# Kernel tuning notes

Measured on AMD Instinct MI355X. Metric: run time of the kernel, lower is better.

The kernel has to match this reference:

```python
import jax, jax.numpy as jnp
import numpy as np

C = 64


def setup_inputs() -> dict:
    key = jax.random.key(0)
    ks = jax.random.split(key, 7)
    x = jax.random.normal(ks[0], (8, C, 64, 64), dtype=jnp.float32)
    # 1x1 conv weights stored as [out_c, in_c]; biases [out_c]
    s = 1.0 / np.sqrt(C)
    W1 = jax.random.uniform(ks[1], (C, C), jnp.float32, -s, s)
    b1 = jax.random.uniform(ks[2], (C,), jnp.float32, -s, s)
    W2 = jax.random.uniform(ks[3], (C, C), jnp.float32, -s, s)
    b2 = jax.random.uniform(ks[4], (C,), jnp.float32, -s, s)
    W3 = jax.random.uniform(ks[5], (C, C), jnp.float32, -s, s)
    b3 = jax.random.uniform(ks[6], (C,), jnp.float32, -s, s)
    return {"x": x, "W1": W1, "b1": b1, "W2": W2, "b2": b2, "W3": W3, "b3": b3}


def reference(x, W1, b1, W2, b2, W3, b3):
    gamma = 1.0
    b, c, h, w = x.shape
    xf = x.reshape(b, c, h * w)  # [b, c, n]
    # 1x1 convs == per-pixel channel matmuls
    f = jnp.einsum('oc,bcn->bon', W1, xf) + b1[None, :, None]
    g = jnp.einsum('oc,bcn->bon', W2, xf) + b2[None, :, None]
    k = jnp.einsum('oc,bcn->bon', W3, xf) + b3[None, :, None]
    # scores[b,i,j] = sum_c f[b,c,i] * g[b,c,j]; softmax over j
    scores = jnp.einsum('bci,bcj->bij', f, g)
    attn = jax.nn.softmax(scores, axis=2)
    # out_attn[b,c,i] = sum_j attn[b,i,j] * k[b,c,j]
    out = jnp.einsum('bij,bcj->bci', attn, k).reshape(b, c, h, w)
    return gamma * out + x
```

## Files before the change

kernel.cpp:

```cpp
#include <hip/hip_runtime.h>
#include <hip/hip_bf16.h>

#define NPIX 4096
#define CCH  64
#define NB   8
#define KVBLK 64

typedef __attribute__((ext_vector_type(8)))  short short8;
typedef __attribute__((ext_vector_type(4)))  float f32x4;
typedef __attribute__((ext_vector_type(16))) float f32x16;

#define LOG2E   1.44269504f

__device__ __forceinline__ unsigned int pack_bf16(float lo, float hi) {
    union { __hip_bfloat162 h; unsigned int u; } w;
    w.h = __float22bfloat162_rn(make_float2(lo, hi));
    return w.u;
}

__global__ __launch_bounds__(256) void proj_kernel(
    const float* __restrict__ x,
    const float* __restrict__ W1, const float* __restrict__ b1,
    const float* __restrict__ W2, const float* __restrict__ b2,
    const float* __restrict__ W3, const float* __restrict__ b3,
    __hip_bfloat16* __restrict__ Q, __hip_bfloat16* __restrict__ G,
    __hip_bfloat16* __restrict__ K)
{
    const int b    = blockIdx.x >> 6;
    const int i0   = (blockIdx.x & 63) << 6;
    const int tid  = threadIdx.x;
    const int wave = tid >> 6;
    const int lane = tid & 63;
    const int l32  = lane & 31;
    const int hi   = lane >> 5;

    __shared__ __hip_bfloat16 Xt[64][72];
    __shared__ __hip_bfloat16 Wb[3][64][64];
    __shared__ float bsh[3][64];

    for (int e = tid; e < 1024; e += 256) {
        const int c = e >> 4, p4 = (e & 15) * 4;
        const f32x4 v = *(const f32x4*)&x[((size_t)b * CCH + c) * NPIX + i0 + p4];
        #pragma unroll
        for (int t = 0; t < 4; ++t)
            Xt[p4 + t][c] = __float2bfloat16(v[t]);
    }
    #pragma unroll
    for (int m = 0; m < 3; ++m) {
        const float* W = (m == 0) ? W1 : (m == 1) ? W2 : W3;
        for (int e = tid; e < 1024; e += 256) {
            const int oc = e >> 4, c4 = (e & 15) * 4;
            const f32x4 v = *(const f32x4*)&W[oc * 64 + c4];
            *(unsigned int*)&Wb[m][oc][c4]     = pack_bf16(v[0], v[1]);
            *(unsigned int*)&Wb[m][oc][c4 + 2] = pack_bf16(v[2], v[3]);
        }
    }
    if (tid < 192) {
        const int m = tid >> 6, oc = tid & 63;
        bsh[m][oc] = ((m == 0) ? b1 : (m == 1) ? b2 : b3)[oc];
    }
    __syncthreads();

    #pragma unroll
    for (int u = 0; u < 3; ++u) {
        const int unit = wave + 4 * u;
        const int m  = unit >> 2;
        const int sr = (unit >> 1) & 1;
        const int sc = unit & 1;

        f32x16 acc;
        #pragma unroll
        for (int r = 0; r < 16; ++r) {
            const int oc = sr * 32 + (r & 3) + 8 * (r >> 2) + 4 * hi;
            acc[r] = bsh[m][oc];
        }
        #pragma unroll
        for (int ks = 0; ks < 4; ++ks) {
            const short8 af = *(const short8*)&Wb[m][sr * 32 + l32][ks * 16 + hi * 8];
            const short8 bf = *(const short8*)&Xt[sc * 32 + l32][ks * 16 + hi * 8];
            acc = __builtin_amdgcn_mfma_f32_32x32x16_bf16(af, bf, acc, 0, 0, 0);
        }

        const int i = i0 + sc * 32 + l32;
        if (m == 0) {
            #pragma unroll
            for (int r = 0; r < 16; ++r) {
                const int oc = sr * 32 + (r & 3) + 8 * (r >> 2) + 4 * hi;
                Q[((size_t)b * NPIX + i) * CCH + oc] = __float2bfloat16(acc[r] * LOG2E);
            }
        } else if (m == 1) {
            #pragma unroll
            for (int r = 0; r < 16; ++r) {
                const int oc = sr * 32 + (r & 3) + 8 * (r >> 2) + 4 * hi;
                G[((size_t)b * NPIX + i) * CCH + oc] = __float2bfloat16(acc[r]);
            }
        } else {
            #pragma unroll
            for (int r = 0; r < 16; ++r) {
                const int oc = sr * 32 + (r & 3) + 8 * (r >> 2) + 4 * hi;
                K[((size_t)b * CCH + oc) * NPIX + i] = __float2bfloat16(acc[r]);
            }
        }
    }
}

__device__ __forceinline__ void gload_lds16(const void* g, void* l) {
    __builtin_amdgcn_global_load_lds(
        (const __attribute__((address_space(1))) unsigned int*)g,
        (__attribute__((address_space(3))) unsigned int*)l, 16, 0, 0);
}

__global__ __launch_bounds__(512, 4) void attn_kernel(
    const __hip_bfloat16* __restrict__ Qg, const __hip_bfloat16* __restrict__ Gg,
    const __hip_bfloat16* __restrict__ Kg,
    __hip_bfloat16* __restrict__ Opart, float* __restrict__ Lpart, int split)
{
    __shared__ char lds[2][16384];

    const int blk   = blockIdx.x;
    const int per_b = 16 * split;
    const int b     = blk / per_b;
    const int rem   = blk - b * per_b;
    const int itile = rem / split;
    const int sp    = rem - itile * split;
    const int tid   = threadIdx.x;
    const int wave  = tid >> 6;
    const int lane  = tid & 63;
    const int l32   = lane & 31;
    const int hi    = lane >> 5;
    const int i0w   = itile * 256 + wave * 32;
    const int jcnt  = NPIX / split;
    const int jlo   = sp * jcnt;
    const int niter = jcnt / KVBLK;

    const short* Qb = (const short*)Qg + (size_t)b * NPIX * CCH;
    const char*  Gb = (const char*)(Gg + (size_t)b * NPIX * CCH);
    const char*  Kb = (const char*)(Kg + (size_t)b * CCH * NPIX);

    short8 q[4];
    #pragma unroll
    for (int ks = 0; ks < 4; ++ks)
        q[ks] = *(const short8*)(Qb + (size_t)(i0w + l32) * CCH + ks * 16 + hi * 8);

    int gbase[2], kbase[2];
    #pragma unroll
    for (int jb = 0; jb < 2; ++jb)
        gbase[jb] = (jb * 32 + l32) * 128 + ((l32 & 7) << 4);
    #pragma unroll
    for (int cb = 0; cb < 2; ++cb)
        kbase[cb] = 8192 + (cb * 32 + l32) * 128 + ((l32 & 7) << 4);

    const int srow = tid >> 3, scolb = (tid & 7) * 16;
    const char* gsrc = Gb + (size_t)(jlo + srow) * 128 + (scolb ^ ((srow & 7) << 4));
    const char* ksrc = Kb + (size_t)srow * 8192 + (size_t)jlo * 2 + (scolb ^ ((srow & 7) << 4));

    f32x16 zacc;
    #pragma unroll
    for (int r = 0; r < 16; ++r) zacc[r] = 0.f;

    f32x16 o[2];
    #pragma unroll
    for (int cb = 0; cb < 2; ++cb)
        #pragma unroll
        for (int r = 0; r < 16; ++r) o[cb][r] = 0.f;
    float ps = 0.f;

    auto STAGE = [&](int buf, int tt) {
        gload_lds16(gsrc + tt * (KVBLK * 128), lds[buf] + wave * 1024);
        gload_lds16(ksrc + tt * (KVBLK * 2),  lds[buf] + 8192 + wave * 1024);
    };

    STAGE(0, 0);
    __syncthreads();

    for (int t = 0; t < niter; ++t) {
        const int cur = t & 1;
        STAGE(cur ^ 1, (t + 1 < niter) ? t + 1 : 0);
        const char* L = lds[cur];

        #pragma unroll
        for (int jb = 0; jb < 2; ++jb) {
            short8 ga[4];
            #pragma unroll
            for (int ks = 0; ks < 4; ++ks)
                ga[ks] = *(const short8*)(L + (gbase[jb] ^ ((2 * ks + hi) << 4)));

            __builtin_amdgcn_s_setprio(1);
            f32x16 acc = __builtin_amdgcn_mfma_f32_32x32x16_bf16(ga[0], q[0], zacc, 0, 0, 0);
            acc = __builtin_amdgcn_mfma_f32_32x32x16_bf16(ga[1], q[1], acc, 0, 0, 0);
            acc = __builtin_amdgcn_mfma_f32_32x32x16_bf16(ga[2], q[2], acc, 0, 0, 0);
            acc = __builtin_amdgcn_mfma_f32_32x32x16_bf16(ga[3], q[3], acc, 0, 0, 0);
            __builtin_amdgcn_s_setprio(0);

            float p[16];
            #pragma unroll
            for (int r = 0; r < 16; ++r) {
                p[r] = __builtin_amdgcn_exp2f(acc[r]);
                ps += p[r];
            }
            short8 pf[2];
            #pragma unroll
            for (int kk = 0; kk < 2; ++kk) {
                unsigned int x0 = pack_bf16(p[8 * kk + 0], p[8 * kk + 1]);
                unsigned int x1 = pack_bf16(p[8 * kk + 2], p[8 * kk + 3]);
                unsigned int y0 = pack_bf16(p[8 * kk + 4], p[8 * kk + 5]);
                unsigned int y1 = pack_bf16(p[8 * kk + 6], p[8 * kk + 7]);
                asm("v_permlane32_swap_b32 %0, %1" : "+v"(x0), "+v"(y0));
                asm("v_permlane32_swap_b32 %0, %1" : "+v"(x1), "+v"(y1));
                union { unsigned int u[4]; short8 v; } w;
                w.u[0] = x0; w.u[1] = x1; w.u[2] = y0; w.u[3] = y1;
                pf[kk] = w.v;
            }

            __builtin_amdgcn_s_setprio(1);
            #pragma unroll
            for (int kk = 0; kk < 2; ++kk) {
                const int ksg = 2 * jb + kk;
                const short8 ka0 = *(const short8*)(L + (kbase[0] ^ ((2 * ksg + hi) << 4)));
                const short8 ka1 = *(const short8*)(L + (kbase[1] ^ ((2 * ksg + hi) << 4)));
                o[0] = __builtin_amdgcn_mfma_f32_32x32x16_bf16(ka0, pf[kk], o[0], 0, 0, 0);
                o[1] = __builtin_amdgcn_mfma_f32_32x32x16_bf16(ka1, pf[kk], o[1], 0, 0, 0);
            }
            __builtin_amdgcn_s_setprio(0);
        }
        __syncthreads();
    }

    const size_t pb = (size_t)(b * split + sp);
    #pragma unroll
    for (int cb = 0; cb < 2; ++cb)
        #pragma unroll
        for (int r = 0; r < 16; ++r) {
            const int c = cb * 32 + (r & 3) + 8 * (r >> 2) + 4 * hi;
            const int i = i0w + l32;
            Opart[(pb * CCH + c) * NPIX + i] = __float2bfloat16(o[cb][r]);
        }
    ps += __shfl_xor(ps, 32);
    if (lane < 32)
        Lpart[pb * NPIX + i0w + l32] = ps;
}

__global__ __launch_bounds__(256) void combine_kernel(
    const __hip_bfloat16* __restrict__ Opart, const float* __restrict__ Lpart,
    const float* __restrict__ x, float* __restrict__ out, int split)
{
    const int b  = blockIdx.x >> 6;
    const int i0 = (blockIdx.x & 63) << 6;

    __shared__ float invL[64];
    if (threadIdx.x < 64) {
        const int i = i0 + threadIdx.x;
        float L = 0.f;
        for (int s = 0; s < split; ++s)
            L += Lpart[((size_t)(b * split + s)) * NPIX + i];
        invL[threadIdx.x] = 1.0f / L;
    }
    __syncthreads();

    const int c    = threadIdx.x >> 2;
    const int ioff = (threadIdx.x & 3) * 16;

    float acc[16];
    #pragma unroll
    for (int k = 0; k < 16; ++k) acc[k] = 0.f;

    for (int s = 0; s < split; ++s) {
        const size_t base = (((size_t)(b * split + s)) * CCH + c) * NPIX + i0 + ioff;
        const short8 v0 = *(const short8*)((const short*)Opart + base);
        const short8 v1 = *(const short8*)((const short*)Opart + base + 8);
        #pragma unroll
        for (int k = 0; k < 8; ++k) {
            union { unsigned int u; float f; } cv0, cv1;
            cv0.u = ((unsigned int)(unsigned short)v0[k]) << 16;
            cv1.u = ((unsigned int)(unsigned short)v1[k]) << 16;
            acc[k]     += cv0.f;
            acc[k + 8] += cv1.f;
        }
    }

    const size_t idx = ((size_t)b * CCH + c) * NPIX + i0 + ioff;
    #pragma unroll
    for (int kq = 0; kq < 4; ++kq) {
        const f32x4 xv = *(const f32x4*)&x[idx + 4 * kq];
        f32x4 r;
        #pragma unroll
        for (int t = 0; t < 4; ++t)
            r[t] = acc[kq * 4 + t] * invL[ioff + kq * 4 + t] + xv[t];
        *(f32x4*)&out[idx + 4 * kq] = r;
    }
}

extern "C" void kernel_launch(void* const* d_in, const int* in_sizes, int n_in,
                              void* d_out, int out_size, void* d_ws, size_t ws_size,
                              hipStream_t stream) {
    const float* x  = (const float*)d_in[0];
    const float* W1 = (const float*)d_in[1];
    const float* b1 = (const float*)d_in[2];
    const float* W2 = (const float*)d_in[3];
    const float* b2 = (const float*)d_in[4];
    const float* W3 = (const float*)d_in[5];
    const float* b3 = (const float*)d_in[6];
    float* out = (float*)d_out;

    char* ws = (char*)d_ws;
    const size_t planeB = (size_t)NB * NPIX * CCH * sizeof(__hip_bfloat16);
    __hip_bfloat16* Q = (__hip_bfloat16*)(ws);
    __hip_bfloat16* G = (__hip_bfloat16*)(ws + planeB);
    __hip_bfloat16* K = (__hip_bfloat16*)(ws + 2 * planeB);

    const size_t base   = 3 * planeB;
    const size_t oPlane = planeB;
    const size_t lPlane = (size_t)NB * NPIX * sizeof(float);

    int split = 8;
    while (split > 1 && base + (size_t)split * (oPlane + lPlane) > ws_size)
        split >>= 1;

    __hip_bfloat16* Opart = (__hip_bfloat16*)(ws + base);
    float* Lpart = (float*)(ws + base + (size_t)split * oPlane);

    proj_kernel<<<dim3(NB * 64), dim3(256), 0, stream>>>(x, W1, b1, W2, b2, W3, b3, Q, G, K);
    attn_kernel<<<dim3(NB * 16 * split), dim3(512), 0, stream>>>(Q, G, K, Opart, Lpart, split);
    combine_kernel<<<dim3(NB * 64), dim3(256), 0, stream>>>(Opart, Lpart, x, out, split);
}
```

Baseline: 73.09 us.

## Load G and K tiles directly from global memory instead of LDS staging

Removes the double-buffered LDS staging of G and K tiles (global_load_lds with swizzled layout) and the per-iteration block barrier. Each wave now reads its MFMA operands straight from global memory, so it relies on L1/L2 caching for reuse across the eight waves of a block. This drops the barrier and the LDS traffic, but adds redundant global loads and exposes global latency with no explicit prefetch.

```diff
diff --git a/kernel.cpp b/kernel.cpp
--- a/kernel.cpp
+++ b/kernel.cpp
@@ -104,19 +104,11 @@
     }
 }
 
-__device__ __forceinline__ void gload_lds16(const void* g, void* l) {
-    __builtin_amdgcn_global_load_lds(
-        (const __attribute__((address_space(1))) unsigned int*)g,
-        (__attribute__((address_space(3))) unsigned int*)l, 16, 0, 0);
-}
-
 __global__ __launch_bounds__(512, 4) void attn_kernel(
     const __hip_bfloat16* __restrict__ Qg, const __hip_bfloat16* __restrict__ Gg,
     const __hip_bfloat16* __restrict__ Kg,
     __hip_bfloat16* __restrict__ Opart, float* __restrict__ Lpart, int split)
 {
-    __shared__ char lds[2][16384];
-
     const int blk   = blockIdx.x;
     const int per_b = 16 * split;
     const int b     = blk / per_b;
@@ -134,25 +126,17 @@
     const int niter = jcnt / KVBLK;
 
     const short* Qb = (const short*)Qg + (size_t)b * NPIX * CCH;
-    const char*  Gb = (const char*)(Gg + (size_t)b * NPIX * CCH);
-    const char*  Kb = (const char*)(Kg + (size_t)b * CCH * NPIX);
+    const short* Gs = (const short*)Gg + (size_t)b * NPIX * CCH;
+    const short* Ks = (const short*)Kg + (size_t)b * CCH * NPIX;
 
     short8 q[4];
     #pragma unroll
     for (int ks = 0; ks < 4; ++ks)
         q[ks] = *(const short8*)(Qb + (size_t)(i0w + l32) * CCH + ks * 16 + hi * 8);
 
-    int gbase[2], kbase[2];
-    #pragma unroll
-    for (int jb = 0; jb < 2; ++jb)
-        gbase[jb] = (jb * 32 + l32) * 128 + ((l32 & 7) << 4);
-    #pragma unroll
-    for (int cb = 0; cb < 2; ++cb)
-        kbase[cb] = 8192 + (cb * 32 + l32) * 128 + ((l32 & 7) << 4);
-
-    const int srow = tid >> 3, scolb = (tid & 7) * 16;
-    const char* gsrc = Gb + (size_t)(jlo + srow) * 128 + (scolb ^ ((srow & 7) << 4));
-    const char* ksrc = Kb + (size_t)srow * 8192 + (size_t)jlo * 2 + (scolb ^ ((srow & 7) << 4));
+    const short* gG = Gs + (size_t)(jlo + l32) * CCH + hi * 8;
+    const short* gK0 = Ks + (size_t)(l32) * NPIX + jlo + hi * 8;
+    const short* gK1 = Ks + (size_t)(32 + l32) * NPIX + jlo + hi * 8;
 
     f32x16 zacc;
     #pragma unroll
@@ -165,25 +149,16 @@
         for (int r = 0; r < 16; ++r) o[cb][r] = 0.f;
     float ps = 0.f;
 
-    auto STAGE = [&](int buf, int tt) {
-        gload_lds16(gsrc + tt * (KVBLK * 128), lds[buf] + wave * 1024);
-        gload_lds16(ksrc + tt * (KVBLK * 2),  lds[buf] + 8192 + wave * 1024);
-    };
-
-    STAGE(0, 0);
-    __syncthreads();
-
     for (int t = 0; t < niter; ++t) {
-        const int cur = t & 1;
-        STAGE(cur ^ 1, (t + 1 < niter) ? t + 1 : 0);
-        const char* L = lds[cur];
+        const int j0 = t * KVBLK;
 
         #pragma unroll
         for (int jb = 0; jb < 2; ++jb) {
+            const short* gr = gG + (size_t)(j0 + jb * 32) * CCH;
             short8 ga[4];
             #pragma unroll
             for (int ks = 0; ks < 4; ++ks)
-                ga[ks] = *(const short8*)(L + (gbase[jb] ^ ((2 * ks + hi) << 4)));
+                ga[ks] = *(const short8*)(gr + ks * 16);
 
             __builtin_amdgcn_s_setprio(1);
             f32x16 acc = __builtin_amdgcn_mfma_f32_32x32x16_bf16(ga[0], q[0], zacc, 0, 0, 0);
@@ -216,14 +191,13 @@
             #pragma unroll
             for (int kk = 0; kk < 2; ++kk) {
                 const int ksg = 2 * jb + kk;
-                const short8 ka0 = *(const short8*)(L + (kbase[0] ^ ((2 * ksg + hi) << 4)));
-                const short8 ka1 = *(const short8*)(L + (kbase[1] ^ ((2 * ksg + hi) << 4)));
+                const short8 ka0 = *(const short8*)(gK0 + j0 + ksg * 16);
+                const short8 ka1 = *(const short8*)(gK1 + j0 + ksg * 16);
                 o[0] = __builtin_amdgcn_mfma_f32_32x32x16_bf16(ka0, pf[kk], o[0], 0, 0, 0);
                 o[1] = __builtin_amdgcn_mfma_f32_32x32x16_bf16(ka1, pf[kk], o[1], 0, 0, 0);
             }
             __builtin_amdgcn_s_setprio(0);
         }
-        __syncthreads();
     }
 
     const size_t pb = (size_t)(b * split + sp);
```

Result: slower. 150.9 us (+106.5%).
